# Optimization experiments

Measured on AMD Instinct MI355X. Metric: run time of the kernel, lower is better.

Reference implementation:

```python
import jax, jax.numpy as jnp
import numpy as np

K_S = 2  # spatial order
K_T = 3  # temporal localization factor


def setup_inputs() -> dict:
    key = jax.random.key(0)
    ks = jax.random.split(key, 5)
    B, T, N = 8, 12, 250
    return {
        "history_data": jax.random.normal(ks[0], (B, T, N, 128), dtype=jnp.float32),
        "Prior": jax.random.normal(ks[1], (B, T, N, 64), dtype=jnp.float32),
        "Observed": jax.random.normal(ks[2], (B, T, N, 32), dtype=jnp.float32),
        "W_emb": jax.random.normal(ks[3], (224, 64), dtype=jnp.float32) * 0.05,
        "b_emb": jnp.zeros((64,), dtype=jnp.float32),
        "use_X": 1,
    }


def _transition(adj):
    # P = D^{-1} A : faithful to diag-embed @ adj, realized as row scaling
    rowsum = adj.sum(axis=-1) + 1e-9
    d_inv = 1.0 / rowsum
    d_inv = jnp.where(jnp.isinf(d_inv) | jnp.isnan(d_inv), 0.0, d_inv)
    return d_inv[..., :, None] * adj


def _forward(history_data, Prior, Observed, W_emb, b_emb):
    # nodevec: [B,T,N,64]
    nodevec = jnp.tanh(
        jnp.concatenate([history_data, Prior, Observed], axis=-1) @ W_emb + b_emb
    )
    # similarity: [B,T,N,N]
    sim = jax.nn.relu(jnp.einsum("btnd,btmd->btnm", nodevec, nodevec))
    # symmetric normalization D^{-1/2} S D^{-1/2}
    d = (sim.sum(axis=-1) + 1e-9) ** -0.5
    adj = d[..., :, None] * sim * d[..., None, :]
    P1 = jnp.swapaxes(_transition(adj), -2, -1)
    P2 = jnp.swapaxes(_transition(jnp.swapaxes(adj, -2, -1)), -2, -1)
    N = adj.shape[-1]
    mask = 1.0 - jnp.eye(N, dtype=adj.dtype)
    outs = []
    for g in (P1, P2):
        k1 = g
        ordered = [k1 * mask]
        for _k in range(2, K_S + 1):
            k1 = k1 @ g
            ordered.append(k1 * mask)
        for og in ordered:
            B, T, Nn, _ = og.shape
            # st_localization: tile each row K_T times along last dim
            ex = jnp.broadcast_to(og[..., None, :], (B, T, Nn, K_T, Nn))
            outs.append(ex.reshape(B, T, Nn, K_T * Nn))
    return tuple(outs)


def reference(history_data, Prior, Observed, W_emb, b_emb, use_X):
    # use_X == 1 path (fc_x_emb on concatenated features)
    return _forward(history_data, Prior, Observed, W_emb, b_emb)
```

## Files before the change

### kernel.cpp

```cpp
#include <hip/hip_runtime.h>
#include <hip/hip_bf16.h>

#define G_N 96
#define N_N 250
#define N_P 256
#define E_N 64
#define OUT_GSTRIDE (250 * 750)
#define OUT_STRIDE  (96 * 250 * 750)

typedef __attribute__((ext_vector_type(4))) float floatx4;
typedef __attribute__((ext_vector_type(2))) float floatx2;
typedef __attribute__((ext_vector_type(8))) short shortx8;
typedef __attribute__((ext_vector_type(4))) short shortx4;

__device__ __forceinline__ float bf2f(unsigned short u) {
    union { unsigned int i; float f; } v; v.i = ((unsigned int)u) << 16; return v.f;
}
__device__ __forceinline__ unsigned short f2bf(float f) {
    union { float f; unsigned int i; } v; v.f = f;
    unsigned int x = v.i;
    return (unsigned short)((x + 0x7fffu + ((x >> 16) & 1u)) >> 16);
}

__global__ __launch_bounds__(256) void k_embed(
    const float* __restrict__ hist, const float* __restrict__ prior,
    const float* __restrict__ obs, const float* __restrict__ Wemb,
    const float* __restrict__ bemb, unsigned short* __restrict__ nvb)
{
    __shared__ __attribute__((aligned(16))) float Xt[32][68];
    __shared__ __attribute__((aligned(16))) float Wl[32][64];
    const int t  = threadIdx.x;
    const int tx = t & 15, ty = t >> 4;
    const int b   = (blockIdx.x & 7) * 48 + (blockIdx.x >> 3);
    const int rr0 = b * 64;
    const int g   = rr0 >> 8;
    const int n0  = rr0 & 255;

    float acc[4][4] = {};

    for (int c = 0; c < 7; ++c) {
        const float* src; int rowlen, off;
        if (c < 4)      { src = hist;  rowlen = 128; off = c << 5; }
        else if (c < 6) { src = prior; rowlen = 64;  off = (c - 4) << 5; }
        else            { src = obs;   rowlen = 32;  off = 0; }
        __syncthreads();
        {
            const int d  = t & 31;
            const int nb = t >> 5;
            #pragma unroll
            for (int p = 0; p < 8; ++p) {
                const int nl = nb + p * 8;
                const int n  = n0 + nl;
                float v = 0.0f;
                if (n < N_N) v = src[(size_t)(g * N_N + n) * rowlen + off + d];
                Xt[d][nl] = v;
            }
        }
        {
            const int e  = t & 63;
            const int db = t >> 6;
            #pragma unroll
            for (int p = 0; p < 8; ++p) {
                const int dl = db + p * 4;
                Wl[dl][e] = Wemb[(c * 32 + dl) * 64 + e];
            }
        }
        __syncthreads();
        #pragma unroll
        for (int k = 0; k < 32; ++k) {
            const float4 av = *(const float4*)&Xt[k][4 * ty];
            const float4 bv = *(const float4*)&Wl[k][4 * tx];
            const float a[4] = {av.x, av.y, av.z, av.w};
            const float b2[4] = {bv.x, bv.y, bv.z, bv.w};
            #pragma unroll
            for (int r = 0; r < 4; ++r)
                #pragma unroll
                for (int cc = 0; cc < 4; ++cc)
                    acc[r][cc] = fmaf(a[r], b2[cc], acc[r][cc]);
        }
    }
    #pragma unroll
    for (int r = 0; r < 4; ++r) {
        const int nl = 4 * ty + r;
        const int n  = n0 + nl;
        unsigned short* d2 = nvb + ((size_t)g * N_P + (n0 + nl)) * E_N + 4 * tx;
        #pragma unroll
        for (int cc = 0; cc < 4; ++cc) {
            float v = 0.0f;
            if (n < N_N) v = tanhf(acc[r][cc] + bemb[4 * tx + cc]);
            d2[cc] = f2bf(v);
        }
    }
}

__global__ __launch_bounds__(256) void k_sim(
    const unsigned short* __restrict__ nvb, unsigned short* __restrict__ Sb,
    float* __restrict__ rowsum)
{
    const int blk = (blockIdx.x & 7) * 192 + (blockIdx.x >> 3);
    const int g   = blk >> 4;
    const int i0  = (blk & 15) << 4;
    const int t    = threadIdx.x;
    const int w    = t >> 6;
    const int lane = t & 63;
    const int m = lane & 15, kg = lane >> 4;

    const shortx8* nvg = (const shortx8*)(nvb + (size_t)g * N_P * E_N);
    const shortx8 a0 = nvg[(i0 + m) * 8 + kg];
    const shortx8 a1 = nvg[(i0 + m) * 8 + 4 + kg];

    floatx4 acc[4];
    const floatx4 zero = {0.f, 0.f, 0.f, 0.f};
    #pragma unroll
    for (int tt = 0; tt < 4; ++tt) {
        const int j = (w << 6) + (tt << 4) + m;
        const shortx8 b0 = nvg[j * 8 + kg];
        const shortx8 b1 = nvg[j * 8 + 4 + kg];
        floatx4 c = zero;
        c = __builtin_amdgcn_mfma_f32_16x16x32_bf16(a0, b0, c, 0, 0, 0);
        c = __builtin_amdgcn_mfma_f32_16x16x32_bf16(a1, b1, c, 0, 0, 0);
        acc[tt] = c;
    }

    float v[4] = {0.f, 0.f, 0.f, 0.f};
    unsigned short* Sg = Sb + (size_t)g * N_P * N_P;
    #pragma unroll
    for (int tt = 0; tt < 4; ++tt) {
        #pragma unroll
        for (int r = 0; r < 4; ++r) {
            float s = acc[tt][r];
            s = s > 0.f ? s : 0.f;
            const int il = (kg << 2) + r;
            const int j  = (w << 6) + (tt << 4) + m;
            Sg[(size_t)(i0 + il) * N_P + j] = f2bf(s);
            v[r] += s;
        }
    }
    #pragma unroll
    for (int r = 0; r < 4; ++r) {
        v[r] += __shfl_xor(v[r], 1);
        v[r] += __shfl_xor(v[r], 2);
        v[r] += __shfl_xor(v[r], 4);
        v[r] += __shfl_xor(v[r], 8);
    }
    __shared__ float rs[4][16];
    if (m == 0) {
        #pragma unroll
        for (int r = 0; r < 4; ++r) rs[w][(kg << 2) + r] = v[r];
    }
    __syncthreads();
    if (t < 16) rowsum[g * N_P + i0 + t] = rs[0][t] + rs[1][t] + rs[2][t] + rs[3][t];
}

__global__ __launch_bounds__(256) void k_trans(
    const unsigned short* __restrict__ Sb, const float* __restrict__ rowsum,
    float* __restrict__ cArr, float* __restrict__ wArr)
{
    const int blk = (blockIdx.x & 7) * 768 + (blockIdx.x >> 3);
    const int g  = blk >> 6;
    const int r0 = (blk & 63) << 2;
    const int t = threadIdx.x;
    const int w = t >> 6, lane = t & 63;
    __shared__ __attribute__((aligned(16))) float dL[N_P];
    dL[t] = rsqrtf(rowsum[g * N_P + t] + 1e-9f);
    __syncthreads();
    const int row = r0 + w;
    const shortx4 sv = *(const shortx4*)(Sb + (size_t)g * N_P * N_P
                                         + (size_t)row * N_P + lane * 4);
    const float4 dv = *(const float4*)&dL[lane * 4];
    float a = bf2f((unsigned short)sv[0]) * dv.x
            + bf2f((unsigned short)sv[1]) * dv.y
            + bf2f((unsigned short)sv[2]) * dv.z
            + bf2f((unsigned short)sv[3]) * dv.w;
    #pragma unroll
    for (int s = 32; s; s >>= 1) a += __shfl_xor(a, s);
    if (lane == 0) {
        const float d = dL[row];
        const float r = 1.0f / (d * a + 1e-9f);
        const float c = r * d;
        cArr[g * N_P + row] = c;
        wArr[g * N_P + row] = c * d;
    }
}

__global__ __launch_bounds__(256) void k_pq(
    const unsigned short* __restrict__ Sb, const float* __restrict__ rowsum,
    const float* __restrict__ cArr, const float* __restrict__ wArr,
    float* __restrict__ out)
{
    const int blk = (blockIdx.x & 7) * 192 + (blockIdx.x >> 3);
    const int g   = blk >> 4;
    const int i0  = (blk & 15) << 4;
    const int t    = threadIdx.x;
    const int w    = t >> 6;
    const int lane = t & 63;
    const int m = lane & 15, kg = lane >> 4;

    __shared__ __attribute__((aligned(16))) unsigned short As[16][40];
    __shared__ __attribute__((aligned(16))) unsigned short Bs[256][40];
    __shared__ __attribute__((aligned(16))) float wL[N_P];
    __shared__ __attribute__((aligned(16))) float cC[N_P];
    __shared__ float dR16[16];
    __shared__ __attribute__((aligned(16))) float qAll[16][260];

    wL[t] = wArr[g * N_P + t];
    cC[t] = cArr[g * N_P + t];
    if (t < 16) dR16[t] = rsqrtf(rowsum[g * N_P + i0 + t] + 1e-9f);
    __syncthreads();

    const unsigned short* Sg = Sb + (size_t)g * N_P * N_P;
    float* o0 = out + (size_t)g * OUT_GSTRIDE;
    float* o1 = o0 + (size_t)OUT_STRIDE;
    float* o2 = o0 + 2 * (size_t)OUT_STRIDE;
    float* o3 = o0 + 3 * (size_t)OUT_STRIDE;
    const int c0 = lane << 2;

    floatx4 acc[4];
    const floatx4 zero = {0.f, 0.f, 0.f, 0.f};
    #pragma unroll
    for (int tt = 0; tt < 4; ++tt) acc[tt] = zero;

    for (int kb = 0; kb < 8; ++kb) {
        __syncthreads();
        if (t < 64) {
            const int row = t >> 2, c4 = t & 3;
            *(uint4*)&As[row][c4 * 8] =
                *(const uint4*)(Sg + (size_t)(i0 + row) * N_P + kb * 32 + c4 * 8);
        }
        #pragma unroll
        for (int q4 = 0; q4 < 4; ++q4) {
            const int u = t + (q4 << 8);
            const int row = u >> 2, c4 = u & 3;
            *(uint4*)&Bs[row][c4 * 8] =
                *(const uint4*)(Sg + (size_t)row * N_P + kb * 32 + c4 * 8);
        }
        __syncthreads();
        const shortx8 a = *(const shortx8*)&As[m][kg << 3];
        const float4 w0 = *(const float4*)&wL[kb * 32 + (kg << 3)];
        const float4 w1 = *(const float4*)&wL[kb * 32 + (kg << 3) + 4];
        const float wv[8] = {w0.x, w0.y, w0.z, w0.w, w1.x, w1.y, w1.z, w1.w};
        shortx8 aw;
        #pragma unroll
        for (int u = 0; u < 8; ++u)
            aw[u] = (short)f2bf(bf2f((unsigned short)a[u]) * wv[u]);
        #pragma unroll
        for (int tt = 0; tt < 4; ++tt) {
            const shortx8 b = *(const shortx8*)&Bs[(w << 6) + (tt << 4) + m][kg << 3];
            acc[tt] = __builtin_amdgcn_mfma_f32_16x16x32_bf16(aw, b, acc[tt], 0, 0, 0);
        }
        {
            const int row = (kb << 1) + (w >> 1);
            const int i   = i0 + row;
            if (i < N_N && c0 < 252) {
                const float dI = dR16[row];
                const shortx4 sv = *(const shortx4*)(Sg + (size_t)i * N_P + c0);
                const float4 cc4 = *(const float4*)&cC[c0];
                const float p0 = (i == c0)     ? 0.f : dI * bf2f((unsigned short)sv[0]) * cc4.x;
                const float p1 = (i == c0 + 1) ? 0.f : dI * bf2f((unsigned short)sv[1]) * cc4.y;
                const float p2 = (i == c0 + 2) ? 0.f : dI * bf2f((unsigned short)sv[2]) * cc4.z;
                const float p3 = (i == c0 + 3) ? 0.f : dI * bf2f((unsigned short)sv[3]) * cc4.w;
                const floatx2 pxy = {p0, p1}, pzw = {p2, p3};
                float* b0 = ((w & 1) ? o2 : o0) + (size_t)i * 750 + c0;
                #pragma unroll
                for (int rep = 0; rep < 3; ++rep) {
                    const int o = rep * 250;
                    *(floatx2*)(b0 + o) = pxy;
                    if (lane < 62) *(floatx2*)(b0 + o + 2) = pzw;
                }
            }
        }
    }

    #pragma unroll
    for (int tt = 0; tt < 4; ++tt) {
        #pragma unroll
        for (int r = 0; r < 4; ++r) {
            const int lrow = (kg << 2) + r;
            const int col  = (w << 6) + (tt << 4) + m;
            float qv = acc[tt][r] * dR16[lrow] * cC[col];
            if (i0 + lrow == col) qv = 0.f;
            qAll[lrow][col] = qv;
        }
    }
    __syncthreads();

    #pragma unroll
    for (int rr = 0; rr < 4; ++rr) {
        const int row = (rr << 2) + w;
        const int i   = i0 + row;
        if (i >= N_N) continue;
        const floatx4 q4 = *(const floatx4*)&qAll[row][c0];
        if (c0 >= 252) continue;
        const floatx2 qxy = {q4[0], q4[1]}, qzw = {q4[2], q4[3]};
        float* b1 = o1 + (size_t)i * 750 + c0;
        float* b3 = o3 + (size_t)i * 750 + c0;
        #pragma unroll
        for (int rep = 0; rep < 3; ++rep) {
            const int o = rep * 250;
            *(floatx2*)(b1 + o) = qxy;
            *(floatx2*)(b3 + o) = qxy;
            if (lane < 62) {
                *(floatx2*)(b1 + o + 2) = qzw;
                *(floatx2*)(b3 + o + 2) = qzw;
            }
        }
    }
}

extern "C" void kernel_launch(void* const* d_in, const int* in_sizes, int n_in,
                              void* d_out, int out_size, void* d_ws, size_t ws_size,
                              hipStream_t stream) {
    const float* hist  = (const float*)d_in[0];
    const float* prior = (const float*)d_in[1];
    const float* obs   = (const float*)d_in[2];
    const float* Wemb  = (const float*)d_in[3];
    const float* bemb  = (const float*)d_in[4];
    float* out = (float*)d_out;

    char* p = (char*)d_ws;
    unsigned short* nvb = (unsigned short*)p; p += (size_t)G_N * N_P * E_N * 2;
    unsigned short* Sb  = (unsigned short*)p; p += (size_t)G_N * N_P * N_P * 2;
    float* rowsum = (float*)p; p += (size_t)G_N * N_P * 4;
    float* cArr   = (float*)p; p += (size_t)G_N * N_P * 4;
    float* wArr   = (float*)p; p += (size_t)G_N * N_P * 4;

    k_embed<<<dim3(G_N * N_P / 64), dim3(256), 0, stream>>>(hist, prior, obs, Wemb, bemb, nvb);
    k_sim  <<<dim3(G_N * 16),       dim3(256), 0, stream>>>(nvb, Sb, rowsum);
    k_trans<<<dim3(G_N * 64),       dim3(256), 0, stream>>>(Sb, rowsum, cArr, wArr);
    k_pq   <<<dim3(G_N * 16),       dim3(256), 0, stream>>>(Sb, rowsum, cArr, wArr, out);
}
```

Baseline: 365.0 us.

## Drop LDS staging in k_pq and interleave Q stores per column tile

The k_pq kernel no longer stages A and B tiles of the similarity matrix through shared memory with per-k-step barriers. Instead it loads the scaled A fragments once into registers and streams B fragments straight from global memory. Q results are written out per 16-column tile through a small double-buffered shared buffer, so the big output stores overlap the remaining MFMA work instead of all happening at the end. This removes the synchronisation and the LDS traffic but adds more global reads, since B rows are now re-read per lane, and a barrier per column tile.

```diff
diff --git a/kernel.cpp b/kernel.cpp
--- a/kernel.cpp
+++ b/kernel.cpp
@@ -196,12 +196,10 @@
     const int lane = t & 63;
     const int m = lane & 15, kg = lane >> 4;
 
-    __shared__ __attribute__((aligned(16))) unsigned short As[16][40];
-    __shared__ __attribute__((aligned(16))) unsigned short Bs[256][40];
     __shared__ __attribute__((aligned(16))) float wL[N_P];
     __shared__ __attribute__((aligned(16))) float cC[N_P];
     __shared__ float dR16[16];
-    __shared__ __attribute__((aligned(16))) float qAll[16][260];
+    __shared__ __attribute__((aligned(16))) float qT[2][16][68];
 
     wL[t] = wArr[g * N_P + t];
     cC[t] = cArr[g * N_P + t];
@@ -215,93 +213,78 @@
     float* o3 = o0 + 3 * (size_t)OUT_STRIDE;
     const int c0 = lane << 2;
 
-    floatx4 acc[4];
-    const floatx4 zero = {0.f, 0.f, 0.f, 0.f};
-    #pragma unroll
-    for (int tt = 0; tt < 4; ++tt) acc[tt] = zero;
-
+    shortx8 aw[8];
+    const unsigned short* aRow = Sg + (size_t)(i0 + m) * N_P + (kg << 3);
+    #pragma unroll
     for (int kb = 0; kb < 8; ++kb) {
-        __syncthreads();
-        if (t < 64) {
-            const int row = t >> 2, c4 = t & 3;
-            *(uint4*)&As[row][c4 * 8] =
-                *(const uint4*)(Sg + (size_t)(i0 + row) * N_P + kb * 32 + c4 * 8);
-        }
-        #pragma unroll
-        for (int q4 = 0; q4 < 4; ++q4) {
-            const int u = t + (q4 << 8);
-            const int row = u >> 2, c4 = u & 3;
-            *(uint4*)&Bs[row][c4 * 8] =
-                *(const uint4*)(Sg + (size_t)row * N_P + kb * 32 + c4 * 8);
-        }
-        __syncthreads();
-        const shortx8 a = *(const shortx8*)&As[m][kg << 3];
+        const shortx8 a = *(const shortx8*)(aRow + kb * 32);
         const float4 w0 = *(const float4*)&wL[kb * 32 + (kg << 3)];
         const float4 w1 = *(const float4*)&wL[kb * 32 + (kg << 3) + 4];
         const float wv[8] = {w0.x, w0.y, w0.z, w0.w, w1.x, w1.y, w1.z, w1.w};
-        shortx8 aw;
         #pragma unroll
         for (int u = 0; u < 8; ++u)
-            aw[u] = (short)f2bf(bf2f((unsigned short)a[u]) * wv[u]);
-        #pragma unroll
-        for (int tt = 0; tt < 4; ++tt) {
-            const shortx8 b = *(const shortx8*)&Bs[(w << 6) + (tt << 4) + m][kg << 3];
-            acc[tt] = __builtin_amdgcn_mfma_f32_16x16x32_bf16(aw, b, acc[tt], 0, 0, 0);
-        }
-        {
-            const int row = (kb << 1) + (w >> 1);
-            const int i   = i0 + row;
-            if (i < N_N && c0 < 252) {
-                const float dI = dR16[row];
-                const shortx4 sv = *(const shortx4*)(Sg + (size_t)i * N_P + c0);
-                const float4 cc4 = *(const float4*)&cC[c0];
-                const float p0 = (i == c0)     ? 0.f : dI * bf2f((unsigned short)sv[0]) * cc4.x;
-                const float p1 = (i == c0 + 1) ? 0.f : dI * bf2f((unsigned short)sv[1]) * cc4.y;
-                const float p2 = (i == c0 + 2) ? 0.f : dI * bf2f((unsigned short)sv[2]) * cc4.z;
-                const float p3 = (i == c0 + 3) ? 0.f : dI * bf2f((unsigned short)sv[3]) * cc4.w;
-                const floatx2 pxy = {p0, p1}, pzw = {p2, p3};
-                float* b0 = ((w & 1) ? o2 : o0) + (size_t)i * 750 + c0;
+            aw[kb][u] = (short)f2bf(bf2f((unsigned short)a[u]) * wv[u]);
+    }
+
+    for (int tt = 0; tt < 4; ++tt) {
+        floatx4 acc = {0.f, 0.f, 0.f, 0.f};
+        const int j = (w << 6) + (tt << 4) + m;
+        const unsigned short* bRow = Sg + (size_t)j * N_P + (kg << 3);
+        #pragma unroll
+        for (int kb = 0; kb < 8; ++kb) {
+            const shortx8 b = *(const shortx8*)(bRow + kb * 32);
+            acc = __builtin_amdgcn_mfma_f32_16x16x32_bf16(aw[kb], b, acc, 0, 0, 0);
+            if (tt == 0) {
+                const int row = (kb << 1) + (w >> 1);
+                const int i   = i0 + row;
+                if (i < N_N && c0 < 252) {
+                    const float dI = dR16[row];
+                    const shortx4 sv = *(const shortx4*)(Sg + (size_t)i * N_P + c0);
+                    const float4 cc4 = *(const float4*)&cC[c0];
+                    const float p0 = (i == c0)     ? 0.f : dI * bf2f((unsigned short)sv[0]) * cc4.x;
+                    const float p1 = (i == c0 + 1) ? 0.f : dI * bf2f((unsigned short)sv[1]) * cc4.y;
+                    const float p2 = (i == c0 + 2) ? 0.f : dI * bf2f((unsigned short)sv[2]) * cc4.z;
+                    const float p3 = (i == c0 + 3) ? 0.f : dI * bf2f((unsigned short)sv[3]) * cc4.w;
+                    const floatx2 pxy = {p0, p1}, pzw = {p2, p3};
+                    float* b0 = ((w & 1) ? o2 : o0) + (size_t)i * 750 + c0;
+                    #pragma unroll
+                    for (int rep = 0; rep < 3; ++rep) {
+                        const int o = rep * 250;
+                        *(floatx2*)(b0 + o) = pxy;
+                        if (lane < 62) *(floatx2*)(b0 + o + 2) = pzw;
+                    }
+                }
+            }
+        }
+
+        const int bsel = tt & 1;
+        #pragma unroll
+        for (int r = 0; r < 4; ++r) {
+            const int lrow = (kg << 2) + r;
+            float qv = acc[r] * dR16[lrow] * cC[j];
+            if (i0 + lrow == j) qv = 0.f;
+            qT[bsel][lrow][(w << 4) + m] = qv;
+        }
+        __syncthreads();
+
+        const int half = lane >> 5;
+        const int cl   = (lane & 31) << 1;
+        const int jj   = ((cl >> 4) << 6) + (tt << 4) + (cl & 15);
+        if (jj + 1 < N_N) {
+            #pragma unroll
+            for (int pr = 0; pr < 2; ++pr) {
+                const int row = w + (half << 2) + (pr << 3);
+                const int i   = i0 + row;
+                if (i >= N_N) continue;
+                const floatx2 qv = *(const floatx2*)&qT[bsel][row][cl];
+                float* b1 = o1 + (size_t)i * 750 + jj;
+                float* b3 = o3 + (size_t)i * 750 + jj;
                 #pragma unroll
                 for (int rep = 0; rep < 3; ++rep) {
                     const int o = rep * 250;
-                    *(floatx2*)(b0 + o) = pxy;
-                    if (lane < 62) *(floatx2*)(b0 + o + 2) = pzw;
+                    *(floatx2*)(b1 + o) = qv;
+                    *(floatx2*)(b3 + o) = qv;
                 }
-            }
-        }
-    }
-
-    #pragma unroll
-    for (int tt = 0; tt < 4; ++tt) {
-        #pragma unroll
-        for (int r = 0; r < 4; ++r) {
-            const int lrow = (kg << 2) + r;
-            const int col  = (w << 6) + (tt << 4) + m;
-            float qv = acc[tt][r] * dR16[lrow] * cC[col];
-            if (i0 + lrow == col) qv = 0.f;
-            qAll[lrow][col] = qv;
-        }
-    }
-    __syncthreads();
-
-    #pragma unroll
-    for (int rr = 0; rr < 4; ++rr) {
-        const int row = (rr << 2) + w;
-        const int i   = i0 + row;
-        if (i >= N_N) continue;
-        const floatx4 q4 = *(const floatx4*)&qAll[row][c0];
-        if (c0 >= 252) continue;
-        const floatx2 qxy = {q4[0], q4[1]}, qzw = {q4[2], q4[3]};
-        float* b1 = o1 + (size_t)i * 750 + c0;
-        float* b3 = o3 + (size_t)i * 750 + c0;
-        #pragma unroll
-        for (int rep = 0; rep < 3; ++rep) {
-            const int o = rep * 250;
-            *(floatx2*)(b1 + o) = qxy;
-            *(floatx2*)(b3 + o) = qxy;
-            if (lane < 62) {
-                *(floatx2*)(b1 + o + 2) = qzw;
-                *(floatx2*)(b3 + o + 2) = qzw;
             }
         }
     }
```

Result: slower. 452.1 us (+23.9%).
